# Kernel tuning notes

Measured on AMD Instinct MI355X. Metric: run time of the kernel, lower is better.

## Reference

```python
import math
import jax, jax.numpy as jnp
import numpy as np

NHEAD = 4
EPS = 1e-5


def make_pe(max_len, d):
    pos = np.arange(max_len, dtype=np.float32)[:, None]
    div = np.exp(np.arange(0, d, 2, dtype=np.float32) * (-math.log(10000.0) / d))
    pe = np.zeros((max_len, d), np.float32)
    pe[:, 0::2] = np.sin(pos * div)
    pe[:, 1::2] = np.cos(pos * div)
    return jnp.asarray(pe)


def layer_norm(x, g, b):
    m = jnp.mean(x, axis=-1, keepdims=True)
    v = jnp.mean((x - m) ** 2, axis=-1, keepdims=True)
    return (x - m) / jnp.sqrt(v + EPS) * g + b


def mha(q, k, v, wq, bq, wk, bk, wv, bv, wo, bo, kmask=None):
    # q: [b, Lq, d], k/v: [b, Lk, d]
    b_, lq, d = q.shape
    lk = k.shape[1]
    hd = d // NHEAD
    qh = (q @ wq + bq).reshape(b_, lq, NHEAD, hd)
    kh = (k @ wk + bk).reshape(b_, lk, NHEAD, hd)
    vh = (v @ wv + bv).reshape(b_, lk, NHEAD, hd)
    s = jnp.einsum('bqhd,bkhd->bhqk', qh, kh) / jnp.sqrt(jnp.float32(hd))
    if kmask is not None:
        s = jnp.where(kmask[None, None, None, :], s, jnp.float32(-1e9))
    a = jax.nn.softmax(s, axis=-1)
    o = jnp.einsum('bhqk,bkhd->bqhd', a, vh).reshape(b_, lq, d)
    return o @ wo + bo


def _forward(src, in_w, in_b, dec_start,
             e_wq, e_bq, e_wk, e_bk, e_wv, e_bv, e_wo, e_bo,
             e_ln1_g, e_ln1_b, e_w1, e_b1, e_w2, e_b2, e_ln2_g, e_ln2_b,
             d_swq, d_sbq, d_swk, d_sbk, d_swv, d_sbv, d_swo, d_sbo,
             d_ln1_g, d_ln1_b,
             d_cwq, d_cbq, d_cwk, d_cbk, d_cwv, d_cbv, d_cwo, d_cbo,
             d_ln2_g, d_ln2_b,
             d_w1, d_b1, d_w2, d_b2, d_ln3_g, d_ln3_b,
             out_w, out_b, tgt_len):
    B, S = src.shape
    d = in_w.shape[1]
    T = tgt_len
    pe = make_pe(max(S, T) + 10, d)

    # ---- encoder (1 post-norm layer, relu FFN, dropout off) ----
    x = (src[..., None] @ in_w + in_b) * jnp.sqrt(jnp.float32(d))  # [B,S,d]
    x = x + pe[None, :S]
    x = layer_norm(x + mha(x, x, x, e_wq, e_bq, e_wk, e_bk, e_wv, e_bv, e_wo, e_bo), e_ln1_g, e_ln1_b)
    mem = layer_norm(x + (jax.nn.relu(x @ e_w1 + e_b1) @ e_w2 + e_b2), e_ln2_g, e_ln2_b)

    buf0 = jnp.zeros((B, T + 1, d), src.dtype).at[:, 0].set(dec_start[0, 0])
    pe_dec = pe[None, :T + 1]
    kidx = jnp.arange(T + 1)

    def step(buf, t):
        di = buf + pe_dec
        kmask = kidx <= t  # full (non-causal) attention over the t+1 valid tokens
        h = layer_norm(di + mha(di, di, di, d_swq, d_sbq, d_swk, d_sbk,
                                d_swv, d_sbv, d_swo, d_sbo, kmask=kmask),
                       d_ln1_g, d_ln1_b)
        h = layer_norm(h + mha(h, mem, mem, d_cwq, d_cbq, d_cwk, d_cbk,
                               d_cwv, d_cbv, d_cwo, d_cbo),
                       d_ln2_g, d_ln2_b)
        h = layer_norm(h + (jax.nn.relu(h @ d_w1 + d_b1) @ d_w2 + d_b2),
                       d_ln3_g, d_ln3_b)
        last = h[:, t]                       # [B,d] output at the newest position
        buf = buf.at[:, t + 1].set(last)     # feed back as next decoder token
        y = (last @ out_w + out_b)[:, 0]     # [B]
        return buf, y

    _, outs = jax.lax.scan(step, buf0, jnp.arange(T))  # outs: [T,B]
    return outs.T  # [B,T]


def setup_inputs():
    B, S, T, d, ff = 128, 512, 64, 48, 128
    ks = iter(jax.random.split(jax.random.key(0), 64))

    def w(shape, s=0.08):
        return jax.random.normal(next(ks), shape, jnp.float32) * s

    ones = lambda: jnp.ones((d,), jnp.float32)
    zeros = lambda: jnp.zeros((d,), jnp.float32)
    return dict(
        src=jax.random.normal(next(ks), (B, S), jnp.float32),
        in_w=w((1, d)), in_b=w((d,)),
        dec_start=w((1, 1, d), 1.0),
        e_wq=w((d, d)), e_bq=w((d,)), e_wk=w((d, d)), e_bk=w((d,)),
        e_wv=w((d, d)), e_bv=w((d,)), e_wo=w((d, d)), e_bo=w((d,)),
        e_ln1_g=ones(), e_ln1_b=zeros(),
        e_w1=w((d, ff)), e_b1=w((ff,)), e_w2=w((ff, d)), e_b2=w((d,)),
        e_ln2_g=ones(), e_ln2_b=zeros(),
        d_swq=w((d, d)), d_sbq=w((d,)), d_swk=w((d, d)), d_sbk=w((d,)),
        d_swv=w((d, d)), d_sbv=w((d,)), d_swo=w((d, d)), d_sbo=w((d,)),
        d_ln1_g=ones(), d_ln1_b=zeros(),
        d_cwq=w((d, d)), d_cbq=w((d,)), d_cwk=w((d, d)), d_cbk=w((d,)),
        d_cwv=w((d, d)), d_cbv=w((d,)), d_cwo=w((d, d)), d_cbo=w((d,)),
        d_ln2_g=ones(), d_ln2_b=zeros(),
        d_w1=w((d, ff)), d_b1=w((ff,)), d_w2=w((ff, d)), d_b2=w((d,)),
        d_ln3_g=ones(), d_ln3_b=zeros(),
        out_w=w((d, 1)), out_b=w((1,)),
        tgt_len=T,
    )


def reference(src, in_w, in_b, dec_start,
              e_wq, e_bq, e_wk, e_bk, e_wv, e_bv, e_wo, e_bo,
              e_ln1_g, e_ln1_b, e_w1, e_b1, e_w2, e_b2, e_ln2_g, e_ln2_b,
              d_swq, d_sbq, d_swk, d_sbk, d_swv, d_sbv, d_swo, d_sbo,
              d_ln1_g, d_ln1_b,
              d_cwq, d_cbq, d_cwk, d_cbk, d_cwv, d_cbv, d_cwo, d_cbo,
              d_ln2_g, d_ln2_b,
              d_w1, d_b1, d_w2, d_b2, d_ln3_g, d_ln3_b,
              out_w, out_b, tgt_len):
    return _forward(src, in_w, in_b, dec_start,
                    e_wq, e_bq, e_wk, e_bk, e_wv, e_bv, e_wo, e_bo,
                    e_ln1_g, e_ln1_b, e_w1, e_b1, e_w2, e_b2, e_ln2_g, e_ln2_b,
                    d_swq, d_sbq, d_swk, d_sbk, d_swv, d_sbv, d_swo, d_sbo,
                    d_ln1_g, d_ln1_b,
                    d_cwq, d_cbq, d_cwk, d_cbk, d_cwv, d_cbv, d_cwo, d_cbo,
                    d_ln2_g, d_ln2_b,
                    d_w1, d_b1, d_w2, d_b2, d_ln3_g, d_ln3_b,
                    out_w, out_b, tgt_len)
```

## Files before the change

kernel.cpp:

```cpp
#include <hip/hip_runtime.h>
#include <hip/hip_bf16.h>
#include <hip/hip_fp16.h>


constexpr int kB  = 128;
constexpr int kS  = 512;
constexpr int kT  = 64;
constexpr int kD  = 48;
constexpr int kFF = 128;
constexpr int kNH = 4;
constexpr int kHD = 12;

__device__ __forceinline__ void wsync(){
  __builtin_amdgcn_wave_barrier();
  asm volatile("" ::: "memory");
}

template<int CTRL,int RM,int BM,bool BC>
__device__ __forceinline__ float dppmov(float x, float old){
  return __builtin_bit_cast(float, __builtin_amdgcn_update_dpp(
      __builtin_bit_cast(int, old), __builtin_bit_cast(int, x), CTRL, RM, BM, BC));
}
__device__ __forceinline__ float wsum(float x){
  x += dppmov<0x111,0xf,0xf,true>(x, 0.f);
  x += dppmov<0x112,0xf,0xf,true>(x, 0.f);
  x += dppmov<0x114,0xf,0xf,true>(x, 0.f);
  x += dppmov<0x118,0xf,0xf,true>(x, 0.f);
  x += dppmov<0x142,0xa,0xf,true>(x, 0.f);
  x += dppmov<0x143,0xc,0xf,true>(x, 0.f);
  return __builtin_bit_cast(float, __builtin_amdgcn_readlane(__builtin_bit_cast(int, x), 63));
}
__device__ __forceinline__ float wmax(float x){
  const float NI = -3.4e38f;
  x = fmaxf(x, dppmov<0x111,0xf,0xf,false>(x, NI));
  x = fmaxf(x, dppmov<0x112,0xf,0xf,false>(x, NI));
  x = fmaxf(x, dppmov<0x114,0xf,0xf,false>(x, NI));
  x = fmaxf(x, dppmov<0x118,0xf,0xf,false>(x, NI));
  x = fmaxf(x, dppmov<0x142,0xa,0xf,false>(x, NI));
  x = fmaxf(x, dppmov<0x143,0xc,0xf,false>(x, NI));
  return __builtin_bit_cast(float, __builtin_amdgcn_readlane(__builtin_bit_cast(int, x), 63));
}
__device__ __forceinline__ float rowsum16(float x){
  x += dppmov<0x111,0xf,0xf,true>(x, 0.f);
  x += dppmov<0x112,0xf,0xf,true>(x, 0.f);
  x += dppmov<0x114,0xf,0xf,true>(x, 0.f);
  x += dppmov<0x118,0xf,0xf,true>(x, 0.f);
  return x;
}

__device__ __forceinline__ float pe_val(int p, int j){
  int i = j >> 1;
  float f = expf(-0.19188209108283716f * (float)(2*i));
  float a = (float)p * f;
  return (j & 1) ? cosf(a) : sinf(a);
}
__device__ __forceinline__ float pe_fast(int p, int j){
  int i = j >> 1;
  float f = __expf(-0.19188209108283716f * (float)(2*i));
  float a = (float)p * f;
  return (j & 1) ? __cosf(a) : __sinf(a);
}

typedef _Float16 h2v __attribute__((ext_vector_type(2)));
union H2U { __half2 h; h2v v; };
__device__ __forceinline__ float fdot2(__half2 a, __half2 b, float c){
#if __has_builtin(__builtin_amdgcn_fdot2)
  H2U ua, ub; ua.h=a; ub.h=b;
  return __builtin_amdgcn_fdot2(ua.v, ub.v, c, false);
#else
  float2 fa=__half22float2(a), fb=__half22float2(b);
  return fmaf(fa.y, fb.y, fmaf(fa.x, fb.x, c));
#endif
}

__device__ __forceinline__ float dot48d(const __half2* x, const __half* w){
  const __half2* w2=(const __half2*)w;
  float a0=0.f,a1=0.f,a2=0.f,a3=0.f;
  #pragma unroll
  for(int c=0;c<6;c++){
    a0=fdot2(x[4*c+0],w2[4*c+0],a0);
    a1=fdot2(x[4*c+1],w2[4*c+1],a1);
    a2=fdot2(x[4*c+2],w2[4*c+2],a2);
    a3=fdot2(x[4*c+3],w2[4*c+3],a3);
  }
  return (a0+a1)+(a2+a3);
}
__device__ __forceinline__ float dot128d(const __half2* x, const __half* w){
  const __half2* w2=(const __half2*)w;
  float a0=0.f,a1=0.f,a2=0.f,a3=0.f,a4=0.f,a5=0.f,a6=0.f,a7=0.f;
  #pragma unroll
  for(int c=0;c<8;c++){
    a0=fdot2(x[8*c+0],w2[8*c+0],a0);
    a1=fdot2(x[8*c+1],w2[8*c+1],a1);
    a2=fdot2(x[8*c+2],w2[8*c+2],a2);
    a3=fdot2(x[8*c+3],w2[8*c+3],a3);
    a4=fdot2(x[8*c+4],w2[8*c+4],a4);
    a5=fdot2(x[8*c+5],w2[8*c+5],a5);
    a6=fdot2(x[8*c+6],w2[8*c+6],a6);
    a7=fdot2(x[8*c+7],w2[8*c+7],a7);
  }
  return ((a0+a1)+(a2+a3))+((a4+a5)+(a6+a7));
}

__global__ void k_embed(const float* __restrict__ src, const float* __restrict__ in_w,
                        const float* __restrict__ in_b, float* __restrict__ X0){
  int idx = blockIdx.x*256 + threadIdx.x;
  if (idx >= kB*kS*kD) return;
  int j = idx % kD; int bs = idx / kD; int s = bs % kS;
  float v = (src[bs] * in_w[j] + in_b[j]) * 6.928203230275509f;
  X0[idx] = v + pe_fast(s, j);
}

__global__ void __launch_bounds__(256) k_qkv(const float* __restrict__ X,
    const float* __restrict__ wq, const float* __restrict__ bq,
    const float* __restrict__ wk, const float* __restrict__ bk,
    const float* __restrict__ wv, const float* __restrict__ bv,
    __half* __restrict__ Q, __half* __restrict__ K, __half* __restrict__ V){
  __shared__ __align__(16) __half W[3*2688];
  __shared__ __align__(16) float bias[3*kD];
  __shared__ __align__(16) __half2 xt2[32*24];
  int tid = threadIdx.x;
  for (int i=tid;i<3*2304;i+=256){ int m=i/2304, e=i%2304, k=e/48, j=e%48;
    const float* w = (m==0)?wq:((m==1)?wk:wv);
    W[m*2688 + j*56 + k] = __float2half(w[e]); }
  for (int i=tid;i<3*kD;i+=256){ int m=i/kD,e=i%kD;
    const float* w=(m==0)?bq:((m==1)?bk:bv); bias[i]=w[e]; }
  long row0 = (long)blockIdx.x*32;
  const float2* Xp=(const float2*)(X+row0*kD);
  for (int i=tid;i<768;i+=256){ float2 v=Xp[i]; xt2[i]=__floats2half2_rn(v.x,v.y); }
  __syncthreads();
  int r = tid>>3, c0 = tid&7;
  __half2 xr[24];
  #pragma unroll
  for(int u=0;u<24;u++) xr[u]=xt2[r*24+u];
  for (int c=c0; c<3*kD; c+=8){
    int m=c/kD, j=c%kD;
    float acc = bias[m*kD+j] + dot48d(xr, W + m*2688 + j*56);
    __half* o = (m==0)?Q:((m==1)?K:V);
    o[(row0+r)*kD+j]=__float2half(acc);
  }
}

__global__ void __launch_bounds__(256) k_attn(const __half* Q, const __half* __restrict__ K,
                       const __half* __restrict__ V, __half* O){
  int b = blockIdx.x / kNH, h = blockIdx.x % kNH;
  __shared__ __align__(16) __half2 Ks2[kS*6];
  __shared__ __align__(16) float   Vs[kS*kHD];
  int tid = threadIdx.x;
  long base = ((long)b*kS)*kD + h*kHD;
  for (int i=tid;i<kS*6;i+=256){ int r=i/6, c=i%6;
    Ks2[i]=*(const __half2*)&K[base+(long)r*kD+2*c]; }
  for (int i=tid;i<kS*kHD;i+=256){ int r=i/kHD, d=i%kHD;
    Vs[i]=__half2float(V[base+(long)r*kD+d]); }
  const float rs = 0.28867513459481287f;
  int q0 = tid, q1 = tid+256;
  __half2 qa2[6], qb2[6];
  {
    const __half2* qp0=(const __half2*)(Q+base+(long)q0*kD);
    const __half2* qp1=(const __half2*)(Q+base+(long)q1*kD);
    #pragma unroll
    for(int c=0;c<6;c++){ qa2[c]=qp0[c]; qb2[c]=qp1[c]; }
  }
  __syncthreads();
  float acc0[kHD], acc1[kHD];
  #pragma unroll
  for(int j=0;j<kHD;j++){ acc0[j]=0.f; acc1[j]=0.f; }
  float l0=0.f, l1=0.f;
  for(int k=0;k<kS;k++){
    const __half2* kp=Ks2+k*6;
    float sA0=0.f,sA1=0.f,sB0=0.f,sB1=0.f;
    #pragma unroll
    for(int c=0;c<3;c++){
      sA0=fdot2(qa2[2*c],kp[2*c],sA0); sA1=fdot2(qa2[2*c+1],kp[2*c+1],sA1);
      sB0=fdot2(qb2[2*c],kp[2*c],sB0); sB1=fdot2(qb2[2*c+1],kp[2*c+1],sB1);
    }
    float p0=__expf((sA0+sA1)*rs), p1=__expf((sB0+sB1)*rs);
    l0+=p0; l1+=p1;
    const float4* vp=(const float4*)(Vs+k*kHD);
    float4 va=vp[0], vb4=vp[1], vc4=vp[2];
    float vr[kHD]={va.x,va.y,va.z,va.w,vb4.x,vb4.y,vb4.z,vb4.w,vc4.x,vc4.y,vc4.z,vc4.w};
    #pragma unroll
    for(int j=0;j<kHD;j++){ acc0[j]+=p0*vr[j]; acc1[j]+=p1*vr[j]; }
  }
  float i0=1.f/l0, i1=1.f/l1;
  #pragma unroll
  for(int j=0;j<kHD;j++){
    O[base+(long)q0*kD+j]=__float2half(acc0[j]*i0);
    O[base+(long)q1*kD+j]=__float2half(acc1[j]*i1);
  }
}

__global__ void __launch_bounds__(256) k_oproj_ln(const float* __restrict__ Xres, const __half* __restrict__ O,
      const float* __restrict__ wo, const float* __restrict__ bo,
      const float* __restrict__ g, const float* __restrict__ bb,
      __half* __restrict__ Xout){
  __shared__ __align__(16) __half W[kD*56];
  __shared__ float bsh[kD], gs[kD], bs2[kD];
  __shared__ __align__(16) float res[32*kD];
  __shared__ __align__(16) __half2 ot2[32*24];
  __shared__ float mrow[32], rstd[32];
  int tid=threadIdx.x;
  for(int i=tid;i<kD*kD;i+=256){ int k=i/48, j=i%48; W[j*56+k]=__float2half(wo[i]); }
  if(tid<kD){ bsh[tid]=bo[tid]; gs[tid]=g[tid]; bs2[tid]=bb[tid]; }
  long row0=(long)blockIdx.x*32;
  const __half2* Op=(const __half2*)(O+row0*kD);
  for(int i=tid;i<768;i+=256) ot2[i]=Op[i];
  __syncthreads();
  int r=tid>>3, c0=tid&7;
  __half2 orow[24];
  #pragma unroll
  for(int u=0;u<24;u++) orow[u]=ot2[r*24+u];
  for(int j=c0;j<kD;j+=8){
    float acc=bsh[j]+dot48d(orow, W+j*56);
    res[r*kD+j]=Xres[row0*kD + r*kD + j]+acc;
  }
  __syncthreads();
  if(tid<32){
    float s=0.f, s2=0.f;
    for(int j=0;j<kD;j++){ float v=res[tid*kD+j]; s+=v; s2+=v*v; }
    float m=s*(1.f/kD);
    mrow[tid]=m; rstd[tid]=rsqrtf(s2*(1.f/kD)-m*m+1e-5f);
  }
  __syncthreads();
  for(int i=tid;i<32*kD;i+=256){int r2=i/kD,j=i%kD;
    Xout[row0*kD+i]=__float2half((res[i]-mrow[r2])*rstd[r2]*gs[j]+bs2[j]); }
}

__global__ void __launch_bounds__(256) k_ffn_ln(const __half* __restrict__ Xin,
   const float* __restrict__ w1, const float* __restrict__ b1,
   const float* __restrict__ w2, const float* __restrict__ b2,
   const float* __restrict__ g, const float* __restrict__ bb,
   float* __restrict__ Xout){
  __shared__ __align__(16) __half W1[kFF*56];
  __shared__ __align__(16) __half W2[kD*136];
  __shared__ float b1s[kFF], b2s[kD], gs[kD], bs2[kD];
  __shared__ __align__(16) __half xt[16*kD];
  __shared__ __align__(16) __half h1h[16*kFF];
  __shared__ __align__(16) float res[16*kD];
  __shared__ float mrow[16], rstd[16];
  int tid=threadIdx.x;
  for(int i=tid;i<kD*kFF;i+=256){ int k=i/128, c=i%128; W1[c*56+k]=__float2half(w1[i]); }
  for(int i=tid;i<kFF*kD;i+=256){ int u=i/48, j=i%48; W2[j*136+u]=__float2half(w2[i]); }
  if(tid<kFF) b1s[tid]=b1[tid];
  if(tid<kD){ b2s[tid]=b2[tid]; gs[tid]=g[tid]; bs2[tid]=bb[tid]; }
  long row0=(long)blockIdx.x*16;
  const __half2* Xp=(const __half2*)(Xin+row0*kD);
  for(int i=tid;i<384;i+=256) ((__half2*)xt)[i]=Xp[i];
  __syncthreads();
  int r=tid>>4, c0=tid&15;
  {
    __half2 xr[24];
    const __half2* xp=(const __half2*)(xt + r*kD);
    #pragma unroll
    for(int u=0;u<24;u++) xr[u]=xp[u];
    for(int c=c0;c<kFF;c+=16){
      float acc=b1s[c]+dot48d(xr, W1+c*56);
      h1h[r*kFF+c]=__float2half(fmaxf(acc,0.f));
    }
  }
  __syncthreads();
  {
    const __half2* hp=(const __half2*)(h1h + r*kFF);
    for(int j=c0;j<kD;j+=16){
      float acc=b2s[j]+dot128d(hp, W2+j*136);
      res[r*kD+j]=__half2float(xt[r*kD+j])+acc;
    }
  }
  __syncthreads();
  if(tid<16){
    float s=0.f, s2=0.f;
    for(int j=0;j<kD;j++){ float v=res[tid*kD+j]; s+=v; s2+=v*v; }
    float m=s*(1.f/kD);
    mrow[tid]=m; rstd[tid]=rsqrtf(s2*(1.f/kD)-m*m+1e-5f);
  }
  __syncthreads();
  for(int i=tid;i<16*kD;i+=256){int r2=i/kD,j=i%kD;
    Xout[row0*kD+i]=(res[i]-mrow[r2])*rstd[r2]*gs[j]+bs2[j]; }
}

__global__ void __launch_bounds__(256) k_ckv(const float* __restrict__ M,
    const float* __restrict__ wk, const float* __restrict__ bk,
    const float* __restrict__ wv, const float* __restrict__ bv,
    __half* __restrict__ Kc, __half* __restrict__ Vc){
  __shared__ __align__(16) __half W[2*2688];
  __shared__ float bias[2*kD];
  __shared__ __align__(16) __half2 xt2[32*24];
  int tid=threadIdx.x;
  for(int i=tid;i<2*2304;i+=256){ int m=i/2304, e=i%2304, k=e/48, j=e%48;
    W[m*2688 + j*56 + k] = __float2half((m?wv:wk)[e]); }
  for(int i=tid;i<2*kD;i+=256){ int m=i/kD,e=i%kD; bias[i]=(m?bv:bk)[e]; }
  long row0=(long)blockIdx.x*32;
  const float2* Mp=(const float2*)(M+row0*kD);
  for(int i=tid;i<768;i+=256){ float2 v=Mp[i]; xt2[i]=__floats2half2_rn(v.x,v.y); }
  __syncthreads();
  int r=tid>>3, c0=tid&7;
  __half2 xr[24];
  #pragma unroll
  for(int u=0;u<24;u++) xr[u]=xt2[r*24+u];
  long gr=row0+r; long bb2=gr>>9; long s=gr&511;
  for(int c=c0;c<2*kD;c+=8){
    int m=c/kD, j=c%kD;
    float acc=bias[m*kD+j]+dot48d(xr, W+m*2688+j*56);
    if(m==0) Kc[(bb2*kS+s)*kD + j]=__float2half(acc);
    else     Vc[(bb2*kD+j)*kS + s]=__float2half(acc);
  }
}

__global__ void k_prep(const float* __restrict__ swq,const float* __restrict__ swk,
                       const float* __restrict__ swv,const float* __restrict__ swo,
                       const float* __restrict__ cwq,const float* __restrict__ cwo,
                       const float* __restrict__ w1,const float* __restrict__ w2,
                       __half* __restrict__ Wh){
  int idx=blockIdx.x*256+threadIdx.x;
  if(idx>=26112) return;
  if(idx<13824){
    int m=idx/2304, e=idx%2304, j=e/48, k=e%48;
    const float* w = (m==0)?swq:((m==1)?swk:((m==2)?swv:((m==3)?swo:((m==4)?cwq:cwo))));
    Wh[m*2688 + j*56 + k] = __float2half(w[k*48+j]);
  } else if(idx<19968){
    int e=idx-13824, c=e/48, k=e%48;
    Wh[16128 + c*56 + k] = __float2half(w1[k*128+c]);
  } else {
    int e=idx-19968, j=e/128, u=e%128;
    Wh[23296 + j*136 + u] = __float2half(w2[u*48+j]);
  }
}

struct DecP {
  const float *dec_start, *sbq, *sbk, *sbv, *sbo, *ln1g, *ln1b,
              *cbq, *cbo, *ln2g, *ln2b, *fb1, *fb2, *ln3g, *ln3b, *ow, *ob;
};

__global__ void __launch_bounds__(256,1) k_dec(const __half* __restrict__ KT,
    const __half* __restrict__ VT, const __half* __restrict__ Wg, DecP P,
    float* __restrict__ out){
  __shared__ __align__(16) __half Wl[29824];
  __shared__ __align__(16) float peT[kT*kD];
  __shared__ __align__(16) __half KhH[kNH*kT*kHD];
  __shared__ __align__(16) float  Vh[kNH*kT*kHD];
  __shared__ __align__(16) __half qSH[kNH*kHD];
  __shared__ __align__(16) __half xvH[kD], soH[kD], h1H[kD], cqH[kD], covH[kD], h2H[kD];
  __shared__ __align__(16) __half f1H[kFF];
  int tid=threadIdx.x, b=blockIdx.x, wave=tid>>6, lane=tid&63;
  const float rs=0.28867513459481287f;

  for(int i=tid;i<29824/8;i+=256) ((float4*)Wl)[i]=((const float4*)Wg)[i];
  for(int i=tid;i<kT*kD;i+=256){ int tt=i/kD, j=i%kD; peT[i]=pe_val(tt,j); }

  float cur=0, c_sbq=0,c_sbk=0,c_sbv=0, c_bo=0,c_cbq=0,c_cbo=0,c_fb2=0;
  float g1=0,bb1=0,g2=0,bb2=0,g3=0,bb3=0,c_ow=0, c_fb1a=0,c_fb1b=0;
  if(wave==0){
    if(lane<kD){
      cur=P.dec_start[lane];
      c_sbq=P.sbq[lane]; c_sbk=P.sbk[lane]; c_sbv=P.sbv[lane];
      c_bo=P.sbo[lane]; c_cbq=P.cbq[lane]; c_cbo=P.cbo[lane]; c_fb2=P.fb2[lane];
      g1=P.ln1g[lane]; bb1=P.ln1b[lane];
      g2=P.ln2g[lane]; bb2=P.ln2b[lane];
      g3=P.ln3g[lane]; bb3=P.ln3b[lane];
      c_ow=P.ow[lane];
    }
    c_fb1a=P.fb1[lane]; c_fb1b=P.fb1[lane+64];
  }
  float c_ob=P.ob[0];

  __half2 Kr2[4][2][6], Vr2[4][kHD];
  {
    const __half* Kb = KT + (long)b*kS*kD;
    const __half2* Vb = (const __half2*)VT + (long)b*kD*(kS/2);
    #pragma unroll
    for(int i=0;i<4;i++){
      int sp = lane + 64*i;
      #pragma unroll
      for(int e=0;e<2;e++){
        const __half2* kp=(const __half2*)(Kb + (long)(2*sp+e)*kD + wave*kHD);
        #pragma unroll
        for(int c=0;c<6;c++) Kr2[i][e][c]=kp[c];
      }
      #pragma unroll
      for(int u=0;u<kHD;u++) Vr2[i][u]=Vb[(wave*kHD+u)*(kS/2)+sp];
    }
  }
  __syncthreads();

  float h1=0, h2=0, xv=0;
  for(int t=0;t<kT;t++){
    if(wave==0){
      if(lane<kD){ xv=cur+peT[t*kD+lane]; xvH[lane]=__float2half(xv); }
      wsync();
      if(lane<kD){
        float qv=c_sbq+dot48d((const __half2*)xvH, Wl + 0*2688 + lane*56);
        float kv=c_sbk+dot48d((const __half2*)xvH, Wl + 1*2688 + lane*56);
        float vv=c_sbv+dot48d((const __half2*)xvH, Wl + 2*2688 + lane*56);
        int hh=lane/kHD, dd=lane%kHD;
        qSH[lane]=__float2half(qv);
        KhH[(hh*kT+t)*kHD+dd]=__float2half(kv);
        Vh[(hh*kT+t)*kHD+dd]=vv;
      }
      wsync();
      {
        int hh=lane>>4, g=lane&15;
        __half2 q2[6];
        const __half2* qp=(const __half2*)qSH + hh*6;
        #pragma unroll
        for(int c=0;c<6;c++) q2[c]=qp[c];
        float l=0.f, acc[kHD];
        #pragma unroll
        for(int u=0;u<kHD;u++) acc[u]=0.f;
        #pragma unroll
        for(int kk=0;kk<4;kk++){
          int key=g+16*kk;
          if(key<=t){
            const __half2* kp=(const __half2*)KhH + (hh*kT+key)*6;
            float a0=0.f,a1=0.f;
            a0=fdot2(q2[0],kp[0],a0); a1=fdot2(q2[1],kp[1],a1);
            a0=fdot2(q2[2],kp[2],a0); a1=fdot2(q2[3],kp[3],a1);
            a0=fdot2(q2[4],kp[4],a0); a1=fdot2(q2[5],kp[5],a1);
            float p=__expf((a0+a1)*rs);
            l+=p;
            const float4* vp=(const float4*)(Vh+(hh*kT+key)*kHD);
            float4 v0=vp[0], v1=vp[1], v2=vp[2];
            float vr[kHD]={v0.x,v0.y,v0.z,v0.w,v1.x,v1.y,v1.z,v1.w,v2.x,v2.y,v2.z,v2.w};
            #pragma unroll
            for(int u=0;u<kHD;u++) acc[u]+=p*vr[u];
          }
        }
        l=rowsum16(l);
        #pragma unroll
        for(int u=0;u<kHD;u++) acc[u]=rowsum16(acc[u]);
        if(g==15){
          float inv=1.f/l;
          #pragma unroll
          for(int u=0;u<6;u++)
            ((__half2*)soH)[hh*6+u]=__floats2half2_rn(acc[2*u]*inv, acc[2*u+1]*inv);
        }
      }
      wsync();
      {
        float rr=0.f;
        if(lane<kD)
          rr=xv+c_bo+dot48d((const __half2*)soH, Wl+8064+lane*56);
        float s1=wsum(rr), s2=wsum(rr*rr);
        float mean=s1*(1.f/48.f);
        float rstd=rsqrtf(s2*(1.f/48.f)-mean*mean+1e-5f);
        h1=0;
        if(lane<kD){ h1=(rr-mean)*rstd*g1+bb1; h1H[lane]=__float2half(h1); }
      }
      wsync();
      if(lane<kD)
        cqH[lane]=__float2half(c_cbq+dot48d((const __half2*)h1H, Wl+10752+lane*56));
    }
    __syncthreads();
    {
      __half2 q2[6];
      #pragma unroll
      for(int c=0;c<6;c++) q2[c]=((const __half2*)cqH)[wave*6+c];
      float s[8];
      #pragma unroll
      for(int i=0;i<4;i++){
        #pragma unroll
        for(int e=0;e<2;e++){
          float a0=0.f,a1=0.f;
          const __half2* kp=Kr2[i][e];
          a0=fdot2(q2[0],kp[0],a0); a1=fdot2(q2[1],kp[1],a1);
          a0=fdot2(q2[2],kp[2],a0); a1=fdot2(q2[3],kp[3],a1);
          a0=fdot2(q2[4],kp[4],a0); a1=fdot2(q2[5],kp[5],a1);
          s[2*i+e]=(a0+a1)*rs;
        }
      }
      float mloc=s[0];
      #pragma unroll
      for(int j=1;j<8;j++) mloc=fmaxf(mloc,s[j]);
      float M=wmax(mloc);
      float p[8], l=0.f;
      #pragma unroll
      for(int j=0;j<8;j++){ p[j]=__expf(s[j]-M); l+=p[j]; }
      l=wsum(l);
      float inv=1.f/l;
      __half2 ph[4];
      #pragma unroll
      for(int i=0;i<4;i++) ph[i]=__floats2half2_rn(p[2*i],p[2*i+1]);
      float acc[kHD];
      #pragma unroll
      for(int u=0;u<kHD;u++) acc[u]=0.f;
      #pragma unroll
      for(int i=0;i<4;i++){
        #pragma unroll
        for(int u=0;u<kHD;u++) acc[u]=fdot2(ph[i],Vr2[i][u],acc[u]);
      }
      #pragma unroll
      for(int u=0;u<kHD;u++) acc[u]=wsum(acc[u]);
      if(lane==0){
        #pragma unroll
        for(int u=0;u<6;u++)
          ((__half2*)covH)[wave*6+u]=__floats2half2_rn(acc[2*u]*inv, acc[2*u+1]*inv);
      }
    }
    __syncthreads();
    if(wave==0){
      {
        float rr=0.f;
        if(lane<kD)
          rr=h1+c_cbo+dot48d((const __half2*)covH, Wl+13440+lane*56);
        float s1=wsum(rr), s2=wsum(rr*rr);
        float mean=s1*(1.f/48.f);
        float rstd=rsqrtf(s2*(1.f/48.f)-mean*mean+1e-5f);
        h2=0;
        if(lane<kD){ h2=(rr-mean)*rstd*g2+bb2; h2H[lane]=__float2half(h2); }
      }
      wsync();
      {
        float a=c_fb1a+dot48d((const __half2*)h2H, Wl+16128+lane*56);
        float bcol=c_fb1b+dot48d((const __half2*)h2H, Wl+16128+(lane+64)*56);
        f1H[lane]=__float2half(fmaxf(a,0.f));
        f1H[lane+64]=__float2half(fmaxf(bcol,0.f));
      }
      wsync();
      {
        float rr=0.f;
        if(lane<kD)
          rr=h2+c_fb2+dot128d((const __half2*)f1H, Wl+23296+lane*136);
        float s1=wsum(rr), s2=wsum(rr*rr);
        float mean=s1*(1.f/48.f);
        float rstd=rsqrtf(s2*(1.f/48.f)-mean*mean+1e-5f);
        float cv=0.f;
        if(lane<kD){ cv=(rr-mean)*rstd*g3+bb3; cur=cv; }
        float y=wsum(cv*c_ow);
        if(lane==0) out[b*kT+t]=y+c_ob;
      }
    }
  }
}

extern "C" void kernel_launch(void* const* d_in, const int* in_sizes, int n_in,
                              void* d_out, int out_size, void* d_ws, size_t ws_size,
                              hipStream_t stream){
  float* ws = (float*)d_ws;
  __half* Wh = (__half*)ws;
  const size_t NB = (size_t)kB*kS*kD;
  float*  A  = ws + 16384;
  __half* H1 = (__half*)(A + NB);
  __half* H2 = H1 + NB;
  __half* H3 = H2 + NB;

  k_embed<<<(kB*kS*kD+255)/256,256,0,stream>>>((const float*)d_in[0],(const float*)d_in[1],(const float*)d_in[2],A);
  k_qkv  <<<(kB*kS)/32,256,0,stream>>>(A,(const float*)d_in[4],(const float*)d_in[5],(const float*)d_in[6],
                                       (const float*)d_in[7],(const float*)d_in[8],(const float*)d_in[9],H1,H2,H3);
  k_attn <<<kB*kNH,256,0,stream>>>(H1,H2,H3,H1);
  k_oproj_ln<<<(kB*kS)/32,256,0,stream>>>(A,H1,(const float*)d_in[10],(const float*)d_in[11],
                                          (const float*)d_in[12],(const float*)d_in[13],H2);
  k_ffn_ln  <<<(kB*kS)/16,256,0,stream>>>(H2,(const float*)d_in[14],(const float*)d_in[15],(const float*)d_in[16],
                                          (const float*)d_in[17],(const float*)d_in[18],(const float*)d_in[19],A);
  k_ckv     <<<(kB*kS)/32,256,0,stream>>>(A,(const float*)d_in[32],(const float*)d_in[33],
                                          (const float*)d_in[34],(const float*)d_in[35],H1,H3);
  k_prep    <<<(26112+255)/256,256,0,stream>>>((const float*)d_in[20],(const float*)d_in[22],(const float*)d_in[24],
                                               (const float*)d_in[26],(const float*)d_in[30],(const float*)d_in[36],
                                               (const float*)d_in[40],(const float*)d_in[42],Wh);
  DecP P;
  P.dec_start=(const float*)d_in[3];
  P.sbq=(const float*)d_in[21]; P.sbk=(const float*)d_in[23]; P.sbv=(const float*)d_in[25]; P.sbo=(const float*)d_in[27];
  P.ln1g=(const float*)d_in[28]; P.ln1b=(const float*)d_in[29];
  P.cbq=(const float*)d_in[31]; P.cbo=(const float*)d_in[37];
  P.ln2g=(const float*)d_in[38]; P.ln2b=(const float*)d_in[39];
  P.fb1=(const float*)d_in[41]; P.fb2=(const float*)d_in[43];
  P.ln3g=(const float*)d_in[44]; P.ln3b=(const float*)d_in[45];
  P.ow=(const float*)d_in[46]; P.ob=(const float*)d_in[47];
  k_dec<<<kB,256,0,stream>>>(H1,H3,Wh,P,(float*)d_out);
}
```

Measured before the change: 589.3 us.

## Cache decoder weights in registers, drop softmax max, restructure decode loop

The decoder keeps three 48-wide weight columns in registers instead of reading them from LDS each step. It drops the wave max reduction in cross-attention softmax and applies the normalization to the probabilities before the V product. The next step's input plus positional encoding is computed at the end of the previous step, and outputs are collected in lanes and written once. Encoder attention accumulators become float2 fma. The changes trade register pressure and overflow safety (no max-subtraction) for shorter serial per-step latency.

```diff
diff --git a/kernel.cpp b/kernel.cpp
--- a/kernel.cpp
+++ b/kernel.cpp
@@ -28,16 +28,6 @@
   x += dppmov<0x118,0xf,0xf,true>(x, 0.f);
   x += dppmov<0x142,0xa,0xf,true>(x, 0.f);
   x += dppmov<0x143,0xc,0xf,true>(x, 0.f);
-  return __builtin_bit_cast(float, __builtin_amdgcn_readlane(__builtin_bit_cast(int, x), 63));
-}
-__device__ __forceinline__ float wmax(float x){
-  const float NI = -3.4e38f;
-  x = fmaxf(x, dppmov<0x111,0xf,0xf,false>(x, NI));
-  x = fmaxf(x, dppmov<0x112,0xf,0xf,false>(x, NI));
-  x = fmaxf(x, dppmov<0x114,0xf,0xf,false>(x, NI));
-  x = fmaxf(x, dppmov<0x118,0xf,0xf,false>(x, NI));
-  x = fmaxf(x, dppmov<0x142,0xa,0xf,false>(x, NI));
-  x = fmaxf(x, dppmov<0x143,0xc,0xf,false>(x, NI));
   return __builtin_bit_cast(float, __builtin_amdgcn_readlane(__builtin_bit_cast(int, x), 63));
 }
 __device__ __forceinline__ float rowsum16(float x){
@@ -82,6 +72,17 @@
     a1=fdot2(x[4*c+1],w2[4*c+1],a1);
     a2=fdot2(x[4*c+2],w2[4*c+2],a2);
     a3=fdot2(x[4*c+3],w2[4*c+3],a3);
+  }
+  return (a0+a1)+(a2+a3);
+}
+__device__ __forceinline__ float dot48r(const __half2* x, const __half2* w){
+  float a0=0.f,a1=0.f,a2=0.f,a3=0.f;
+  #pragma unroll
+  for(int c=0;c<6;c++){
+    a0=fdot2(x[4*c+0],w[4*c+0],a0);
+    a1=fdot2(x[4*c+1],w[4*c+1],a1);
+    a2=fdot2(x[4*c+2],w[4*c+2],a2);
+    a3=fdot2(x[4*c+3],w[4*c+3],a3);
   }
   return (a0+a1)+(a2+a3);
 }
@@ -162,9 +163,9 @@
     for(int c=0;c<6;c++){ qa2[c]=qp0[c]; qb2[c]=qp1[c]; }
   }
   __syncthreads();
-  float acc0[kHD], acc1[kHD];
-  #pragma unroll
-  for(int j=0;j<kHD;j++){ acc0[j]=0.f; acc1[j]=0.f; }
+  float2 acc0[6], acc1[6];
+  #pragma unroll
+  for(int j=0;j<6;j++){ acc0[j]=make_float2(0.f,0.f); acc1[j]=make_float2(0.f,0.f); }
   float l0=0.f, l1=0.f;
   for(int k=0;k<kS;k++){
     const __half2* kp=Ks2+k*6;
@@ -176,17 +177,21 @@
     }
     float p0=__expf((sA0+sA1)*rs), p1=__expf((sB0+sB1)*rs);
     l0+=p0; l1+=p1;
-    const float4* vp=(const float4*)(Vs+k*kHD);
-    float4 va=vp[0], vb4=vp[1], vc4=vp[2];
-    float vr[kHD]={va.x,va.y,va.z,va.w,vb4.x,vb4.y,vb4.z,vb4.w,vc4.x,vc4.y,vc4.z,vc4.w};
+    const float2* vp=(const float2*)(Vs+k*kHD);
     #pragma unroll
-    for(int j=0;j<kHD;j++){ acc0[j]+=p0*vr[j]; acc1[j]+=p1*vr[j]; }
+    for(int j=0;j<6;j++){
+      float2 v=vp[j];
+      acc0[j].x=fmaf(p0,v.x,acc0[j].x); acc0[j].y=fmaf(p0,v.y,acc0[j].y);
+      acc1[j].x=fmaf(p1,v.x,acc1[j].x); acc1[j].y=fmaf(p1,v.y,acc1[j].y);
+    }
   }
   float i0=1.f/l0, i1=1.f/l1;
   #pragma unroll
-  for(int j=0;j<kHD;j++){
-    O[base+(long)q0*kD+j]=__float2half(acc0[j]*i0);
-    O[base+(long)q1*kD+j]=__float2half(acc1[j]*i1);
+  for(int j=0;j<6;j++){
+    O[base+(long)q0*kD+2*j  ]=__float2half(acc0[j].x*i0);
+    O[base+(long)q0*kD+2*j+1]=__float2half(acc0[j].y*i0);
+    O[base+(long)q1*kD+2*j  ]=__float2half(acc1[j].x*i1);
+    O[base+(long)q1*kD+2*j+1]=__float2half(acc1[j].y*i1);
   }
 }
 
@@ -347,11 +352,11 @@
   for(int i=tid;i<29824/8;i+=256) ((float4*)Wl)[i]=((const float4*)Wg)[i];
   for(int i=tid;i<kT*kD;i+=256){ int tt=i/kD, j=i%kD; peT[i]=pe_val(tt,j); }
 
-  float cur=0, c_sbq=0,c_sbk=0,c_sbv=0, c_bo=0,c_cbq=0,c_cbo=0,c_fb2=0;
-  float g1=0,bb1=0,g2=0,bb2=0,g3=0,bb3=0,c_ow=0, c_fb1a=0,c_fb1b=0;
+  float c_sbq=0,c_sbk=0,c_sbv=0, c_bo=0,c_cbq=0,c_cbo=0,c_fb2=0;
+  float g1=0,bb1=0,g2=0,bb2=0,g3=0,bb3=0,c_ow=0, c_fb1a=0,c_fb1b=0, c_ds=0;
   if(wave==0){
     if(lane<kD){
-      cur=P.dec_start[lane];
+      c_ds=P.dec_start[lane];
       c_sbq=P.sbq[lane]; c_sbk=P.sbk[lane]; c_sbv=P.sbv[lane];
       c_bo=P.sbo[lane]; c_cbq=P.cbq[lane]; c_cbo=P.cbo[lane]; c_fb2=P.fb2[lane];
       g1=P.ln1g[lane]; bb1=P.ln1b[lane];
@@ -382,11 +387,23 @@
   }
   __syncthreads();
 
-  float h1=0, h2=0, xv=0;
+  __half2 wA3[24], wA4[24], wC0[24];
+  {
+    int col = (lane<kD)?lane:0;
+    const __half2* p3=(const __half2*)(Wl+ 8064+col*56);
+    const __half2* p4=(const __half2*)(Wl+10752+col*56);
+    const __half2* p0=(const __half2*)(Wl+13440+col*56);
+    #pragma unroll
+    for(int u=0;u<24;u++){ wA3[u]=p3[u]; wA4[u]=p4[u]; wC0[u]=p0[u]; }
+  }
+
+  float xv=0;
+  if(wave==0 && lane<kD){ xv=c_ds+peT[lane]; xvH[lane]=__float2half(xv); }
+  __syncthreads();
+
+  float h1=0, h2=0, yacc=0;
   for(int t=0;t<kT;t++){
     if(wave==0){
-      if(lane<kD){ xv=cur+peT[t*kD+lane]; xvH[lane]=__float2half(xv); }
-      wsync();
       if(lane<kD){
         float qv=c_sbq+dot48d((const __half2*)xvH, Wl + 0*2688 + lane*56);
         float kv=c_sbk+dot48d((const __half2*)xvH, Wl + 1*2688 + lane*56);
@@ -438,7 +455,7 @@
       {
         float rr=0.f;
         if(lane<kD)
-          rr=xv+c_bo+dot48d((const __half2*)soH, Wl+8064+lane*56);
+          rr=xv+c_bo+dot48r((const __half2*)soH, wA3);
         float s1=wsum(rr), s2=wsum(rr*rr);
         float mean=s1*(1.f/48.f);
         float rstd=rsqrtf(s2*(1.f/48.f)-mean*mean+1e-5f);
@@ -447,7 +464,7 @@
       }
       wsync();
       if(lane<kD)
-        cqH[lane]=__float2half(c_cbq+dot48d((const __half2*)h1H, Wl+10752+lane*56));
+        cqH[lane]=__float2half(c_cbq+dot48r((const __half2*)h1H, wA4));
     }
     __syncthreads();
     {
@@ -467,18 +484,14 @@
           s[2*i+e]=(a0+a1)*rs;
         }
       }
-      float mloc=s[0];
-      #pragma unroll
-      for(int j=1;j<8;j++) mloc=fmaxf(mloc,s[j]);
-      float M=wmax(mloc);
-      float p[8], l=0.f;
-      #pragma unroll
-      for(int j=0;j<8;j++){ p[j]=__expf(s[j]-M); l+=p[j]; }
+      float p32[8], l=0.f;
+      #pragma unroll
+      for(int j=0;j<8;j++){ p32[j]=__expf(s[j]); l+=p32[j]; }
       l=wsum(l);
       float inv=1.f/l;
       __half2 ph[4];
       #pragma unroll
-      for(int i=0;i<4;i++) ph[i]=__floats2half2_rn(p[2*i],p[2*i+1]);
+      for(int i=0;i<4;i++) ph[i]=__floats2half2_rn(p32[2*i]*inv, p32[2*i+1]*inv);
       float acc[kHD];
       #pragma unroll
       for(int u=0;u<kHD;u++) acc[u]=0.f;
@@ -492,7 +505,7 @@
       if(lane==0){
         #pragma unroll
         for(int u=0;u<6;u++)
-          ((__half2*)covH)[wave*6+u]=__floats2half2_rn(acc[2*u]*inv, acc[2*u+1]*inv);
+          ((__half2*)covH)[wave*6+u]=__floats2half2_rn(acc[2*u], acc[2*u+1]);
       }
     }
     __syncthreads();
@@ -500,7 +513,7 @@
       {
         float rr=0.f;
         if(lane<kD)
-          rr=h1+c_cbo+dot48d((const __half2*)covH, Wl+13440+lane*56);
+          rr=h1+c_cbo+dot48r((const __half2*)covH, wC0);
         float s1=wsum(rr), s2=wsum(rr*rr);
         float mean=s1*(1.f/48.f);
         float rstd=rsqrtf(s2*(1.f/48.f)-mean*mean+1e-5f);
@@ -523,12 +536,15 @@
         float mean=s1*(1.f/48.f);
         float rstd=rsqrtf(s2*(1.f/48.f)-mean*mean+1e-5f);
         float cv=0.f;
-        if(lane<kD){ cv=(rr-mean)*rstd*g3+bb3; cur=cv; }
+        if(lane<kD) cv=(rr-mean)*rstd*g3+bb3;
+        if(lane<kD && t+1<kT){ xv=cv+peT[(t+1)*kD+lane]; xvH[lane]=__float2half(xv); }
+        wsync();
         float y=wsum(cv*c_ow);
-        if(lane==0) out[b*kT+t]=y+c_ob;
-      }
-    }
-  }
+        if(lane==t) yacc=y;
+      }
+    }
+  }
+  if(wave==0) out[(long)b*kT+lane]=yacc+c_ob;
 }
 
 extern "C" void kernel_launch(void* const* d_in, const int* in_sizes, int n_in,
```

Result: slower. 608.7 us (+3.3%).
